# Kernel optimization log

Hardware: AMD Instinct MI355X
Metric: run time of the kernel (lower is better)

Reference implementation:

```python
import jax, jax.numpy as jnp
import numpy as np

STATE = 16
DT_RANK = 48
INNER = 1536
LN_EPS = 1e-5


def setup_inputs() -> dict:
    key = jax.random.key(0)
    ks = jax.random.split(key, 10)
    B, C, H, W = 128, 2048, 24, 12
    hid = 768
    inp = {}
    inp["x"] = jax.random.normal(ks[0], (B, C, H, W), jnp.float32)
    inp["pe_w"] = jax.random.normal(ks[1], (C, hid), jnp.float32) * 0.02
    inp["pe_b"] = jnp.zeros((hid,), jnp.float32)
    inp["ln_g"] = jnp.ones((hid,), jnp.float32)
    inp["ln_b"] = jnp.zeros((hid,), jnp.float32)
    inp["in_w"] = jax.random.normal(ks[2], (hid, 2 * INNER), jnp.float32) * 0.02
    inp["conv_w"] = jax.random.normal(ks[3], (INNER, 1, 3), jnp.float32) * 0.1
    inp["conv_b"] = jnp.zeros((INNER,), jnp.float32)
    # faithful init: A = repeat(arange(1, state+1)), A_log = log(A)
    inp["A_log"] = jnp.log(jnp.broadcast_to(jnp.arange(1, STATE + 1, dtype=jnp.float32), (INNER, STATE)))
    inp["xproj_w"] = jax.random.normal(ks[4], (INNER, DT_RANK + 2 * STATE), jnp.float32) * 0.02
    inp["dtproj_w"] = jax.random.normal(ks[5], (DT_RANK, INNER), jnp.float32) * 0.02
    inp["dtproj_b"] = jnp.zeros((INNER,), jnp.float32)
    inp["D_param"] = jnp.ones((INNER,), jnp.float32)
    inp["out_w"] = jax.random.normal(ks[6], (INNER, C), jnp.float32) * 0.02
    return inp


def _forward(x, pe_w, pe_b, ln_g, ln_b, in_w, conv_w, conv_b, A_log,
             xproj_w, dtproj_w, dtproj_b, D_param, out_w):
    B, C, H, W = x.shape
    # Patch_Embedding: AdaptiveAvgPool2d((3,3)) -- H,W divisible by 3 -> block mean
    xp = x.reshape(B, C, 3, H // 3, 3, W // 3).mean(axis=(3, 5))  # [B,C,3,3]
    tok = xp.reshape(B, C, 9).transpose(0, 2, 1)                   # [B,9,C]
    tok = tok @ pe_w + pe_b                                        # [B,9,hid]

    # Mamba: LayerNorm (biased variance)
    mu = tok.mean(-1, keepdims=True)
    var = tok.var(-1, keepdims=True)
    h = (tok - mu) / jnp.sqrt(var + LN_EPS) * ln_g + ln_b

    xz = h @ in_w                                                  # [B,9,2*inner]
    xs, z = xz[..., :INNER], xz[..., INNER:]

    # depthwise conv1d, kernel 3, pad 1
    xc = jax.lax.conv_general_dilated(
        xs.transpose(0, 2, 1), conv_w, window_strides=(1,), padding=[(1, 1)],
        feature_group_count=INNER, dimension_numbers=("NCH", "OIH", "NCH"))
    xc = (xc + conv_b[None, :, None]).transpose(0, 2, 1)           # [B,9,inner]
    xc = jax.nn.silu(xc)

    # SSM selective scan
    A = -jnp.exp(A_log)                                            # [inner,state]
    dbc = xc @ xproj_w                                             # [B,9,dtr+2*state]
    d_r = dbc[..., :DT_RANK]
    Bp = dbc[..., DT_RANK:DT_RANK + STATE]                         # [B,9,state]
    Cp = dbc[..., DT_RANK + STATE:]                                # [B,9,state]
    delta = jax.nn.softplus(d_r @ dtproj_w + dtproj_b)             # [B,9,inner]

    dA = jnp.exp(delta[..., None] * A)                             # [B,9,inner,state]
    dBu = delta[..., None] * Bp[:, :, None, :] * xc[..., None]     # [B,9,inner,state]

    def step(s, t):
        dA_i, dBu_i, C_i = t                                       # [B,inner,state],[B,inner,state],[B,state]
        s = dA_i * s + dBu_i
        y = jnp.einsum("bdn,bn->bd", s, C_i)
        return s, y

    s0 = jnp.zeros((B, INNER, STATE), xc.dtype)
    _, ys = jax.lax.scan(step, s0, (dA.transpose(1, 0, 2, 3),
                                    dBu.transpose(1, 0, 2, 3),
                                    Cp.transpose(1, 0, 2)))
    y = ys.transpose(1, 0, 2) + xc * D_param                       # [B,9,inner]

    y = y * jax.nn.silu(z)
    out = y @ out_w                                                # [B,9,C]

    # Inverse_Patch_Embedding: reshape to [B,C,3,3], bilinear upsample (align_corners=False)
    out = out.transpose(0, 2, 1).reshape(B, C, 3, 3)
    out = jax.image.resize(out, (B, C, H, W), method="bilinear")
    return out


def reference(x, pe_w, pe_b, ln_g, ln_b, in_w, conv_w, conv_b, A_log,
              xproj_w, dtproj_w, dtproj_b, D_param, out_w):
    return _forward(x, pe_w, pe_b, ln_g, ln_b, in_w, conv_w, conv_b, A_log,
                    xproj_w, dtproj_w, dtproj_b, D_param, out_w)
```

## Files before the change

### kernel.cpp

```cpp
#include <hip/hip_runtime.h>
#include <math.h>

#define Bn   128
#define Cn   2048
#define Hn   24
#define Wn   12
#define HID  768
#define NIN  1536
#define NST  16
#define DTR  48
#define Ln   9
#define Mn   (Bn*Ln)
#define XKS  16

typedef __bf16 bf16x8 __attribute__((ext_vector_type(8)));
typedef float  f32x4  __attribute__((ext_vector_type(4)));

#define GLOAD16(gsrc, ldst) \
  __builtin_amdgcn_global_load_lds((const __attribute__((address_space(1))) void*)(gsrc), \
                                   (__attribute__((address_space(3))) void*)(ldst), 16, 0, 0)

__device__ __forceinline__ unsigned short f2bf(float f) {
  unsigned u = __float_as_uint(f);
  u += 0x7fffu + ((u >> 16) & 1u);
  return (unsigned short)(u >> 16);
}
__device__ __forceinline__ float bf2f(unsigned short h) {
  return __uint_as_float(((unsigned)h) << 16);
}
__device__ __forceinline__ void split_bf(float f, unsigned short& hi, unsigned short& lo) {
  hi = f2bf(f);
  lo = f2bf(f - bf2f(hi));
}
__device__ __forceinline__ int col2(int k) { return ((k >> 5) << 6) + (k & 31); }

__global__ __launch_bounds__(256) void prep_kernel(const float* __restrict__ pe_w,
    const float* __restrict__ in_w, const float* __restrict__ out_w,
    const float* __restrict__ x,
    unsigned short* __restrict__ peT2, unsigned short* __restrict__ inT2,
    unsigned short* __restrict__ outT2, unsigned short* __restrict__ tok2) {
  __shared__ char smem[32 * 73 * 16];
  int bid = blockIdx.x;
  int t = threadIdx.x;
  if (bid < 6912) {
    float (*tile)[33] = reinterpret_cast<float (*)[33]>(smem);
    const float* W; unsigned short* T2; int K, N, nb, kb;
    if (bid < 1536)      { W = pe_w;  T2 = peT2;  K = Cn;  N = HID;     nb = bid % 24; kb = bid / 24; }
    else if (bid < 3840) { int q = bid - 1536; W = in_w;  T2 = inT2;  K = HID; N = 2 * NIN; nb = q % 96; kb = q / 96; }
    else                 { int q = bid - 3840; W = out_w; T2 = outT2; K = NIN; N = Cn;      nb = q % 64; kb = q / 64; }
    int kl = t >> 3, n4 = (t & 7) * 4;
    float4 v = *reinterpret_cast<const float4*>(W + (size_t)(kb * 32 + kl) * N + nb * 32 + n4);
    tile[kl][n4] = v.x; tile[kl][n4 + 1] = v.y; tile[kl][n4 + 2] = v.z; tile[kl][n4 + 3] = v.w;
    __syncthreads();
    int nl = t >> 3, k4 = (t & 7) * 4;
    unsigned short hi[4], lo[4];
    #pragma unroll
    for (int i = 0; i < 4; ++i) split_bf(tile[k4 + i][nl], hi[i], lo[i]);
    size_t base = (size_t)(nb * 32 + nl) * (2 * K) + kb * 64 + k4;
    uint2 ph, pl;
    ph.x = (unsigned)hi[0] | ((unsigned)hi[1] << 16);
    ph.y = (unsigned)hi[2] | ((unsigned)hi[3] << 16);
    pl.x = (unsigned)lo[0] | ((unsigned)lo[1] << 16);
    pl.y = (unsigned)lo[2] | ((unsigned)lo[3] << 16);
    *reinterpret_cast<uint2*>(T2 + base)      = ph;
    *reinterpret_cast<uint2*>(T2 + base + 32) = pl;
  } else {
    float4 (*raw)[73] = reinterpret_cast<float4 (*)[73]>(smem);
    int blk = bid - 6912;
    int b = blk >> 6, cg = blk & 63;
    const float4* src = reinterpret_cast<const float4*>(x) + (size_t)(b * Cn + cg * 32) * 72;
    #pragma unroll
    for (int it = 0; it < 9; ++it) {
      int li = it * 256 + t;
      raw[li / 72][li % 72] = src[li];
    }
    __syncthreads();
    for (int cell = t; cell < 288; cell += 256) {
      int c = cell / 9, p = cell % 9, i = p / 3, j = p % 3;
      float s = 0.f;
      #pragma unroll
      for (int k = 0; k < 8; ++k) {
        float4 v = raw[c][(i * 8 + k) * 3 + j];
        s += (v.x + v.y) + (v.z + v.w);
      }
      s *= (1.0f / 32.0f);
      unsigned short hi, lo;
      split_bf(s, hi, lo);
      int cglob = cg * 32 + c;
      size_t base = ((size_t)(b * Ln + p)) * (2 * Cn) + col2(cglob);
      tok2[base] = hi; tok2[base + 32] = lo;
    }
  }
}

__global__ __launch_bounds__(256) void mgemm_kernel(
    const unsigned short* __restrict__ A2, const unsigned short* __restrict__ B2,
    float* __restrict__ Cout, int M, int N, int K, int Ksub) {
  __shared__ unsigned short As[2][128][64];
  __shared__ unsigned short Bs[2][128][64];
  int t = threadIdx.x;
  int bm = blockIdx.y * 128, bn = blockIdx.x * 128;
  int wave = t >> 6, lane = t & 63;
  int wr = (wave >> 1) * 64, wc = (wave & 1) * 64;
  int lr = lane & 15, lk = lane >> 4;

  int l3 = lane >> 3, c8 = lane & 7;
  int sc = c8 ^ l3;
  size_t koff = (size_t)blockIdx.z * 2 * (size_t)Ksub;
  const unsigned short* Ab = A2 + (size_t)(bm + wave * 32 + l3) * (2 * (size_t)K) + koff + sc * 8;
  const unsigned short* Bb = B2 + (size_t)(bn + wave * 32 + l3) * (2 * (size_t)K) + koff + sc * 8;
  size_t rstep = (size_t)8 * 2 * K;

  f32x4 acc[4][4];
  #pragma unroll
  for (int m = 0; m < 4; ++m)
    #pragma unroll
    for (int n = 0; n < 4; ++n) acc[m][n] = {0.f, 0.f, 0.f, 0.f};

  {
    unsigned short* AsW = &As[0][wave * 32][0];
    unsigned short* BsW = &Bs[0][wave * 32][0];
    #pragma unroll
    for (int q = 0; q < 4; ++q) {
      GLOAD16(Ab + q * rstep, AsW + q * 8 * 64);
      GLOAD16(Bb + q * rstep, BsW + q * 8 * 64);
    }
  }
  __syncthreads();

  int cur = 0;
  for (int kk = 0; kk < Ksub; kk += 32) {
    if (kk + 32 < Ksub) {
      unsigned short* AsW = &As[cur ^ 1][wave * 32][0];
      unsigned short* BsW = &Bs[cur ^ 1][wave * 32][0];
      #pragma unroll
      for (int q = 0; q < 4; ++q) {
        GLOAD16(Ab + q * rstep + (kk + 32) * 2, AsW + q * 8 * 64);
        GLOAD16(Bb + q * rstep + (kk + 32) * 2, BsW + q * 8 * 64);
      }
    }

    bf16x8 ah[4], al[4], bh[4], bl[4];
    #pragma unroll
    for (int m = 0; m < 4; ++m) {
      int ar = wr + m * 16 + lr;
      ah[m] = *reinterpret_cast<const bf16x8*>(&As[cur][ar][((lk    ) ^ (ar & 7)) * 8]);
      al[m] = *reinterpret_cast<const bf16x8*>(&As[cur][ar][((4 + lk) ^ (ar & 7)) * 8]);
    }
    #pragma unroll
    for (int n = 0; n < 4; ++n) {
      int br = wc + n * 16 + lr;
      bh[n] = *reinterpret_cast<const bf16x8*>(&Bs[cur][br][((lk    ) ^ (br & 7)) * 8]);
      bl[n] = *reinterpret_cast<const bf16x8*>(&Bs[cur][br][((4 + lk) ^ (br & 7)) * 8]);
    }
    #pragma unroll
    for (int m = 0; m < 4; ++m)
      #pragma unroll
      for (int n = 0; n < 4; ++n) {
        acc[m][n] = __builtin_amdgcn_mfma_f32_16x16x32_bf16(ah[m], bh[n], acc[m][n], 0, 0, 0);
        acc[m][n] = __builtin_amdgcn_mfma_f32_16x16x32_bf16(ah[m], bl[n], acc[m][n], 0, 0, 0);
        acc[m][n] = __builtin_amdgcn_mfma_f32_16x16x32_bf16(al[m], bh[n], acc[m][n], 0, 0, 0);
      }
    __syncthreads();
    cur ^= 1;
  }

  float* dst = Cout + (size_t)blockIdx.z * M * N;
  #pragma unroll
  for (int m = 0; m < 4; ++m)
    #pragma unroll
    for (int n = 0; n < 4; ++n) {
      int col = bn + wc + n * 16 + lr;
      #pragma unroll
      for (int r = 0; r < 4; ++r) {
        int row = bm + wr + m * 16 + lk * 4 + r;
        dst[(size_t)row * N + col] = acc[m][n][r];
      }
    }
}

__global__ __launch_bounds__(256) void xproj_kernel(const float* __restrict__ xc,
    const float* __restrict__ w, float* __restrict__ part) {
  __shared__ float at[64][44];
  __shared__ float wt[32][80];
  int kc = blockIdx.x, mt = blockIdx.y;
  int t = threadIdx.x;
  int tx = t & 15, ty = t >> 4;
  float acc[4][5] = {};
  int sr = t >> 3, sc4 = (t & 7) * 4;
  for (int k0 = kc * 96; k0 < kc * 96 + 96; k0 += 32) {
    __syncthreads();
    float4 v0 = *reinterpret_cast<const float4*>(xc + (size_t)(mt * 64 + sr) * NIN + k0 + sc4);
    float4 v1 = *reinterpret_cast<const float4*>(xc + (size_t)(mt * 64 + sr + 32) * NIN + k0 + sc4);
    *reinterpret_cast<float4*>(&at[sr][sc4])      = v0;
    *reinterpret_cast<float4*>(&at[sr + 32][sc4]) = v1;
    for (int i = t; i < 32 * 80; i += 256)
      wt[i / 80][i % 80] = w[(size_t)(k0 + i / 80) * 80 + i % 80];
    __syncthreads();
    #pragma unroll
    for (int kk = 0; kk < 32; ++kk) {
      float a0[4], b0[5];
      #pragma unroll
      for (int i = 0; i < 4; ++i) a0[i] = at[ty * 4 + i][kk];
      #pragma unroll
      for (int j = 0; j < 5; ++j) b0[j] = wt[kk][tx + 16 * j];
      #pragma unroll
      for (int i = 0; i < 4; ++i)
        #pragma unroll
        for (int j = 0; j < 5; ++j)
          acc[i][j] = fmaf(a0[i], b0[j], acc[i][j]);
    }
  }
  #pragma unroll
  for (int i = 0; i < 4; ++i)
    #pragma unroll
    for (int j = 0; j < 5; ++j)
      part[((size_t)kc * Mn + mt * 64 + ty * 4 + i) * 80 + tx + 16 * j] = acc[i][j];
}

__global__ __launch_bounds__(256) void ln_kernel(const float* __restrict__ part1,
    const float* __restrict__ peb, const float* __restrict__ g, const float* __restrict__ be,
    unsigned short* __restrict__ h2) {
  int row = blockIdx.x;
  int t = threadIdx.x;
  float vq[3];
  #pragma unroll
  for (int q = 0; q < 3; ++q) {
    int c = t + q * 256;
    float v = peb[c];
    #pragma unroll
    for (int ks = 0; ks < 8; ++ks)
      v += part1[((size_t)ks * Mn + row) * HID + c];
    vq[q] = v;
  }
  float s  = vq[0] + vq[1] + vq[2];
  float s2 = vq[0] * vq[0] + vq[1] * vq[1] + vq[2] * vq[2];
  #pragma unroll
  for (int o = 32; o > 0; o >>= 1) {
    s  += __shfl_down(s,  o, 64);
    s2 += __shfl_down(s2, o, 64);
  }
  __shared__ float red[8];
  int wid = t >> 6, lane = t & 63;
  if (lane == 0) { red[wid] = s; red[4 + wid] = s2; }
  __syncthreads();
  float S  = red[0] + red[1] + red[2] + red[3];
  float S2 = red[4] + red[5] + red[6] + red[7];
  float mu  = S * (1.0f / HID);
  float var = S2 * (1.0f / HID) - mu * mu;
  float inv = rsqrtf(var + 1e-5f);
  #pragma unroll
  for (int q = 0; q < 3; ++q) {
    int c = t + q * 256;
    float hv = (vq[q] - mu) * inv * g[c] + be[c];
    unsigned short hi, lo;
    split_bf(hv, hi, lo);
    size_t base = (size_t)row * (2 * HID) + col2(c);
    h2[base] = hi; h2[base + 32] = lo;
  }
}

__global__ __launch_bounds__(256) void conv_silu_kernel(const float* __restrict__ part2,
    const float* __restrict__ w, const float* __restrict__ cb, float* __restrict__ xc) {
  int idx = blockIdx.x * 256 + threadIdx.x;
  if (idx >= Mn * NIN) return;
  int d  = idx % NIN;
  int bp = idx / NIN;
  int p = bp % Ln, b = bp / Ln;
  const float* pa = part2 + (size_t)(b * Ln) * (2 * NIN) + d;
  const float* pb = pa + (size_t)Mn * 2 * NIN;
  float acc = cb[d];
  float w0 = w[d * 3], w1 = w[d * 3 + 1], w2 = w[d * 3 + 2];
  if (p > 0) {
    size_t o1 = (size_t)(p - 1) * (2 * NIN);
    acc += (pa[o1] + pb[o1]) * w0;
  }
  size_t o2 = (size_t)p * (2 * NIN);
  acc += (pa[o2] + pb[o2]) * w1;
  if (p < Ln - 1) {
    size_t o3 = (size_t)(p + 1) * (2 * NIN);
    acc += (pa[o3] + pb[o3]) * w2;
  }
  float sg = 1.0f / (1.0f + expf(-acc));
  xc[idx] = acc * sg;
}

__global__ __launch_bounds__(256) void scan_kernel(const float* __restrict__ partx,
    const float* __restrict__ xcb, const float* __restrict__ A_log,
    const float* __restrict__ Dp, const float* __restrict__ part2,
    const float* __restrict__ dtw, const float* __restrict__ dtb,
    unsigned short* __restrict__ ya2) {
  __shared__ float wdt[DTR * 256];
  __shared__ float dbc9[Ln][DTR];
  __shared__ float Bsh[Ln][NST], Csh[Ln][NST];
  int b      = blockIdx.x / (NIN / 256);
  int dchunk = blockIdx.x % (NIN / 256);
  int t = threadIdx.x;
  float4* w4 = reinterpret_cast<float4*>(wdt);
  #pragma unroll
  for (int it = 0; it < 12; ++it) {
    int i4 = it * 256 + t;
    int k = i4 >> 6, c4 = i4 & 63;
    w4[i4] = *reinterpret_cast<const float4*>(dtw + (size_t)k * NIN + dchunk * 256 + c4 * 4);
  }
  for (int i = t; i < Ln * 80; i += 256) {
    int p = i / 80, k = i - p * 80;
    size_t off = (size_t)(b * Ln + p) * 80 + k;
    float s = 0.f;
    #pragma unroll
    for (int ks = 0; ks < XKS; ++ks) s += partx[(size_t)ks * (Mn * 80) + off];
    if (k < DTR)            dbc9[p][k] = s;
    else if (k < DTR + NST) Bsh[p][k - DTR] = s;
    else                    Csh[p][k - DTR - NST] = s;
  }
  __syncthreads();
  int d = dchunk * 256 + t;
  float Ar[NST];
  #pragma unroll
  for (int n = 0; n < NST; ++n) Ar[n] = -expf(A_log[(size_t)d * NST + n]);
  float s[NST];
  #pragma unroll
  for (int n = 0; n < NST; ++n) s[n] = 0.0f;
  float Dv = Dp[d];
  float bt = dtb[d];
  int cc = col2(d);
  const float* z0 = part2 + NIN + d;
  const float* z1 = z0 + (size_t)Mn * 2 * NIN;
  for (int p = 0; p < Ln; ++p) {
    size_t off = (size_t)(b * Ln + p) * NIN + d;
    float a = bt;
    #pragma unroll
    for (int k = 0; k < DTR; ++k) a = fmaf(dbc9[p][k], wdt[k * 256 + t], a);
    float dl = fmaxf(a, 0.0f) + log1pf(expf(-fabsf(a)));
    float u  = xcb[off];
    float du = dl * u;
    float y = 0.0f;
    #pragma unroll
    for (int n = 0; n < NST; ++n) {
      float dA = expf(dl * Ar[n]);
      s[n] = dA * s[n] + du * Bsh[p][n];
      y += s[n] * Csh[p][n];
    }
    size_t zoff = (size_t)(b * Ln + p) * (2 * NIN);
    float zv = z0[zoff] + z1[zoff];
    float sz = zv / (1.0f + expf(-zv));
    float yv = (y + u * Dv) * sz;
    unsigned short hi, lo;
    split_bf(yv, hi, lo);
    size_t base = (size_t)(b * Ln + p) * (2 * NIN) + cc;
    ya2[base] = hi; ya2[base + 32] = lo;
  }
}

__global__ __launch_bounds__(256) void resize_kernel(const float* __restrict__ part3,
                                                     float* __restrict__ out) {
  __shared__ float v[32][10];
  int blk = blockIdx.x;
  int b = blk >> 6, cg = blk & 63;
  int t = threadIdx.x;
  size_t MN3 = (size_t)Mn * Cn;
  for (int i = t; i < 288; i += 256) {
    int p = i >> 5, c = i & 31;
    size_t base = (size_t)(b * Ln + p) * Cn + cg * 32 + c;
    v[c][p] = part3[base] + part3[base + MN3] + part3[base + 2 * MN3] + part3[base + 3 * MN3];
  }
  __syncthreads();
  int ch = t >> 3, sub = t & 7;
  float* dst = out + ((size_t)b * Cn + cg * 32 + ch) * 288;
  #pragma unroll
  for (int q = 0; q < 9; ++q) {
    int f = sub + q * 8;
    int y = f / 3, xq = f - y * 3;
    float fy  = (y + 0.5f) * 0.125f - 0.5f;
    float fyf = floorf(fy);
    float wy  = fy - fyf;
    int yy = (int)fyf;
    int y0 = min(2, max(0, yy)), y1 = min(2, max(0, yy + 1));
    float rr[3];
    #pragma unroll
    for (int j = 0; j < 3; ++j)
      rr[j] = v[ch][y0 * 3 + j] * (1.0f - wy) + v[ch][y1 * 3 + j] * wy;
    float ov[4];
    #pragma unroll
    for (int xi = 0; xi < 4; ++xi) {
      int xo = xq * 4 + xi;
      float fx  = (xo + 0.5f) * 0.25f - 0.5f;
      float fxf = floorf(fx);
      float wx  = fx - fxf;
      int xx = (int)fxf;
      int x0 = min(2, max(0, xx)), x1 = min(2, max(0, xx + 1));
      ov[xi] = rr[x0] * (1.0f - wx) + rr[x1] * wx;
    }
    *reinterpret_cast<float4*>(dst + f * 4) = make_float4(ov[0], ov[1], ov[2], ov[3]);
  }
}

extern "C" void kernel_launch(void* const* d_in, const int* in_sizes, int n_in,
                              void* d_out, int out_size, void* d_ws, size_t ws_size,
                              hipStream_t stream) {
  const float* x        = (const float*)d_in[0];
  const float* pe_w     = (const float*)d_in[1];
  const float* pe_b     = (const float*)d_in[2];
  const float* ln_g     = (const float*)d_in[3];
  const float* ln_b     = (const float*)d_in[4];
  const float* in_w     = (const float*)d_in[5];
  const float* conv_w   = (const float*)d_in[6];
  const float* conv_b   = (const float*)d_in[7];
  const float* A_log    = (const float*)d_in[8];
  const float* xproj_w  = (const float*)d_in[9];
  const float* dtproj_w = (const float*)d_in[10];
  const float* dtproj_b = (const float*)d_in[11];
  const float* D_param  = (const float*)d_in[12];
  const float* out_w    = (const float*)d_in[13];
  float* out = (float*)d_out;
  char* ws = (char*)d_ws;

  size_t o = 0;
  auto alloc = [&](size_t bytes) { size_t r = o; o += (bytes + 255) & ~(size_t)255; return r; };
  unsigned short* tok2  = (unsigned short*)(ws + alloc((size_t)Mn * 2 * Cn * 2));
  unsigned short* peT2  = (unsigned short*)(ws + alloc((size_t)HID * 2 * Cn * 2));
  unsigned short* inT2  = (unsigned short*)(ws + alloc((size_t)2 * NIN * 2 * HID * 2));
  unsigned short* outT2 = (unsigned short*)(ws + alloc((size_t)Cn * 2 * NIN * 2));
  unsigned short* h2    = (unsigned short*)(ws + alloc((size_t)Mn * 2 * HID * 2));
  unsigned short* ya2   = (unsigned short*)(ws + alloc((size_t)Mn * 2 * NIN * 2));
  float* xc    = (float*)(ws + alloc((size_t)Mn * NIN * 4));
  float* part1 = (float*)(ws + alloc((size_t)8 * Mn * HID * 4));
  float* part2 = (float*)(ws + alloc((size_t)2 * Mn * 2 * NIN * 4));
  float* part3 = (float*)(ws + alloc((size_t)4 * Mn * Cn * 4));
  float* partx = (float*)(ws + alloc((size_t)XKS * Mn * 80 * 4));

  prep_kernel<<<15104, 256, 0, stream>>>(pe_w, in_w, out_w, x, peT2, inT2, outT2, tok2);

  mgemm_kernel<<<dim3(HID / 128, Mn / 128, 8), 256, 0, stream>>>(
      tok2, peT2, part1, Mn, HID, Cn, Cn / 8);
  ln_kernel<<<Mn, 256, 0, stream>>>(part1, pe_b, ln_g, ln_b, h2);
  mgemm_kernel<<<dim3(2 * NIN / 128, Mn / 128, 2), 256, 0, stream>>>(
      h2, inT2, part2, Mn, 2 * NIN, HID, HID / 2);
  conv_silu_kernel<<<(Mn * NIN) / 256, 256, 0, stream>>>(part2, conv_w, conv_b, xc);
  xproj_kernel<<<dim3(XKS, Mn / 64), 256, 0, stream>>>(xc, xproj_w, partx);
  scan_kernel<<<Bn * (NIN / 256), 256, 0, stream>>>(
      partx, xc, A_log, D_param, part2, dtproj_w, dtproj_b, ya2);
  mgemm_kernel<<<dim3(Cn / 128, Mn / 128, 4), 256, 0, stream>>>(
      ya2, outT2, part3, Mn, Cn, NIN, NIN / 4);
  resize_kernel<<<Bn * (Cn / 32), 256, 0, stream>>>(part3, out);
}
```

Before: 312.3 us.

## Fuse depthwise conv+SiLU into xproj and scan, halve out-proj split-K

Removes the standalone conv_silu kernel and its xc buffer. The depthwise conv and SiLU are now recomputed on the fly from the in-projection partials, both inside the xproj GEMM tile loader and inside the scan kernel, which slides a three-tap window along the sequence. It also switches expf to __expf in the scan, and reduces the output GEMM split-K from 4 to 2, which shrinks the partial buffer the resize kernel reads. The cost is redundant conv work and extra partial-buffer reads in xproj and scan, plus fewer blocks for the output GEMM.

```diff
diff --git a/kernel.cpp b/kernel.cpp
--- a/kernel.cpp
+++ b/kernel.cpp
@@ -179,7 +179,42 @@
     }
 }
 
-__global__ __launch_bounds__(256) void xproj_kernel(const float* __restrict__ xc,
+__device__ __forceinline__ float4 conv_silu4(const float* __restrict__ p0,
+    const float* __restrict__ p1, const float* __restrict__ cw,
+    const float* __restrict__ cb, int R, int d0) {
+  int bq = R / 9, pq = R - bq * 9;
+  size_t rb = (size_t)R * (2 * NIN) + d0;
+  float4 a0 = *reinterpret_cast<const float4*>(p0 + rb);
+  float4 a1 = *reinterpret_cast<const float4*>(p1 + rb);
+  float cx[4] = {a0.x + a1.x, a0.y + a1.y, a0.z + a1.z, a0.w + a1.w};
+  float cm[4] = {0.f, 0.f, 0.f, 0.f}, cp[4] = {0.f, 0.f, 0.f, 0.f};
+  if (pq > 0) {
+    float4 m0 = *reinterpret_cast<const float4*>(p0 + rb - 2 * NIN);
+    float4 m1 = *reinterpret_cast<const float4*>(p1 + rb - 2 * NIN);
+    cm[0] = m0.x + m1.x; cm[1] = m0.y + m1.y; cm[2] = m0.z + m1.z; cm[3] = m0.w + m1.w;
+  }
+  if (pq < Ln - 1) {
+    float4 q0 = *reinterpret_cast<const float4*>(p0 + rb + 2 * NIN);
+    float4 q1 = *reinterpret_cast<const float4*>(p1 + rb + 2 * NIN);
+    cp[0] = q0.x + q1.x; cp[1] = q0.y + q1.y; cp[2] = q0.z + q1.z; cp[3] = q0.w + q1.w;
+  }
+  float4 w0 = *reinterpret_cast<const float4*>(cw + 3 * d0);
+  float4 w1 = *reinterpret_cast<const float4*>(cw + 3 * d0 + 4);
+  float4 w2 = *reinterpret_cast<const float4*>(cw + 3 * d0 + 8);
+  float wf[12] = {w0.x, w0.y, w0.z, w0.w, w1.x, w1.y, w1.z, w1.w, w2.x, w2.y, w2.z, w2.w};
+  float4 cb4 = *reinterpret_cast<const float4*>(cb + d0);
+  float cbf[4] = {cb4.x, cb4.y, cb4.z, cb4.w};
+  float r[4];
+  #pragma unroll
+  for (int i = 0; i < 4; ++i) {
+    float a = cbf[i] + cm[i] * wf[3 * i] + cx[i] * wf[3 * i + 1] + cp[i] * wf[3 * i + 2];
+    r[i] = a / (1.0f + __expf(-a));
+  }
+  return make_float4(r[0], r[1], r[2], r[3]);
+}
+
+__global__ __launch_bounds__(256) void xproj_kernel(const float* __restrict__ part2,
+    const float* __restrict__ cw, const float* __restrict__ cb,
     const float* __restrict__ w, float* __restrict__ part) {
   __shared__ float at[64][44];
   __shared__ float wt[32][80];
@@ -188,10 +223,12 @@
   int tx = t & 15, ty = t >> 4;
   float acc[4][5] = {};
   int sr = t >> 3, sc4 = (t & 7) * 4;
+  const float* p0 = part2;
+  const float* p1 = part2 + (size_t)Mn * 2 * NIN;
   for (int k0 = kc * 96; k0 < kc * 96 + 96; k0 += 32) {
+    float4 v0 = conv_silu4(p0, p1, cw, cb, mt * 64 + sr,      k0 + sc4);
+    float4 v1 = conv_silu4(p0, p1, cw, cb, mt * 64 + sr + 32, k0 + sc4);
     __syncthreads();
-    float4 v0 = *reinterpret_cast<const float4*>(xc + (size_t)(mt * 64 + sr) * NIN + k0 + sc4);
-    float4 v1 = *reinterpret_cast<const float4*>(xc + (size_t)(mt * 64 + sr + 32) * NIN + k0 + sc4);
     *reinterpret_cast<float4*>(&at[sr][sc4])      = v0;
     *reinterpret_cast<float4*>(&at[sr + 32][sc4]) = v1;
     for (int i = t; i < 32 * 80; i += 256)
@@ -260,36 +297,11 @@
   }
 }
 
-__global__ __launch_bounds__(256) void conv_silu_kernel(const float* __restrict__ part2,
-    const float* __restrict__ w, const float* __restrict__ cb, float* __restrict__ xc) {
-  int idx = blockIdx.x * 256 + threadIdx.x;
-  if (idx >= Mn * NIN) return;
-  int d  = idx % NIN;
-  int bp = idx / NIN;
-  int p = bp % Ln, b = bp / Ln;
-  const float* pa = part2 + (size_t)(b * Ln) * (2 * NIN) + d;
-  const float* pb = pa + (size_t)Mn * 2 * NIN;
-  float acc = cb[d];
-  float w0 = w[d * 3], w1 = w[d * 3 + 1], w2 = w[d * 3 + 2];
-  if (p > 0) {
-    size_t o1 = (size_t)(p - 1) * (2 * NIN);
-    acc += (pa[o1] + pb[o1]) * w0;
-  }
-  size_t o2 = (size_t)p * (2 * NIN);
-  acc += (pa[o2] + pb[o2]) * w1;
-  if (p < Ln - 1) {
-    size_t o3 = (size_t)(p + 1) * (2 * NIN);
-    acc += (pa[o3] + pb[o3]) * w2;
-  }
-  float sg = 1.0f / (1.0f + expf(-acc));
-  xc[idx] = acc * sg;
-}
-
 __global__ __launch_bounds__(256) void scan_kernel(const float* __restrict__ partx,
-    const float* __restrict__ xcb, const float* __restrict__ A_log,
-    const float* __restrict__ Dp, const float* __restrict__ part2,
-    const float* __restrict__ dtw, const float* __restrict__ dtb,
-    unsigned short* __restrict__ ya2) {
+    const float* __restrict__ A_log, const float* __restrict__ Dp,
+    const float* __restrict__ part2, const float* __restrict__ dtw,
+    const float* __restrict__ dtb, const float* __restrict__ cw,
+    const float* __restrict__ cb, unsigned short* __restrict__ ya2) {
   __shared__ float wdt[DTR * 256];
   __shared__ float dbc9[Ln][DTR];
   __shared__ float Bsh[Ln][NST], Csh[Ln][NST];
@@ -317,38 +329,47 @@
   int d = dchunk * 256 + t;
   float Ar[NST];
   #pragma unroll
-  for (int n = 0; n < NST; ++n) Ar[n] = -expf(A_log[(size_t)d * NST + n]);
+  for (int n = 0; n < NST; ++n) Ar[n] = -__expf(A_log[(size_t)d * NST + n]);
   float s[NST];
   #pragma unroll
   for (int n = 0; n < NST; ++n) s[n] = 0.0f;
   float Dv = Dp[d];
   float bt = dtb[d];
+  float w0 = cw[3 * d], w1 = cw[3 * d + 1], w2 = cw[3 * d + 2];
+  float cbv = cb[d];
   int cc = col2(d);
-  const float* z0 = part2 + NIN + d;
-  const float* z1 = z0 + (size_t)Mn * 2 * NIN;
+  const float* px0 = part2 + d;
+  const float* px1 = px0 + (size_t)Mn * 2 * NIN;
+  const float* z0  = part2 + NIN + d;
+  const float* z1  = z0 + (size_t)Mn * 2 * NIN;
+  size_t row0 = (size_t)(b * Ln) * (2 * NIN);
+  float xm = 0.f;
+  float x0 = px0[row0] + px1[row0];
   for (int p = 0; p < Ln; ++p) {
-    size_t off = (size_t)(b * Ln + p) * NIN + d;
+    size_t roff = row0 + (size_t)p * (2 * NIN);
+    float xp = 0.f;
+    if (p < Ln - 1) xp = px0[roff + 2 * NIN] + px1[roff + 2 * NIN];
+    float a0 = cbv + xm * w0 + x0 * w1 + xp * w2;
+    float u = a0 / (1.0f + __expf(-a0));
     float a = bt;
     #pragma unroll
     for (int k = 0; k < DTR; ++k) a = fmaf(dbc9[p][k], wdt[k * 256 + t], a);
-    float dl = fmaxf(a, 0.0f) + log1pf(expf(-fabsf(a)));
-    float u  = xcb[off];
+    float dl = fmaxf(a, 0.0f) + log1pf(__expf(-fabsf(a)));
     float du = dl * u;
     float y = 0.0f;
     #pragma unroll
     for (int n = 0; n < NST; ++n) {
-      float dA = expf(dl * Ar[n]);
+      float dA = __expf(dl * Ar[n]);
       s[n] = dA * s[n] + du * Bsh[p][n];
       y += s[n] * Csh[p][n];
     }
-    size_t zoff = (size_t)(b * Ln + p) * (2 * NIN);
-    float zv = z0[zoff] + z1[zoff];
-    float sz = zv / (1.0f + expf(-zv));
+    float zv = z0[roff] + z1[roff];
+    float sz = zv / (1.0f + __expf(-zv));
     float yv = (y + u * Dv) * sz;
     unsigned short hi, lo;
     split_bf(yv, hi, lo);
-    size_t base = (size_t)(b * Ln + p) * (2 * NIN) + cc;
-    ya2[base] = hi; ya2[base + 32] = lo;
+    ya2[roff + cc] = hi; ya2[roff + cc + 32] = lo;
+    xm = x0; x0 = xp;
   }
 }
 
@@ -362,7 +383,7 @@
   for (int i = t; i < 288; i += 256) {
     int p = i >> 5, c = i & 31;
     size_t base = (size_t)(b * Ln + p) * Cn + cg * 32 + c;
-    v[c][p] = part3[base] + part3[base + MN3] + part3[base + 2 * MN3] + part3[base + 3 * MN3];
+    v[c][p] = part3[base] + part3[base + MN3];
   }
   __syncthreads();
   int ch = t >> 3, sub = t & 7;
@@ -423,10 +444,9 @@
   unsigned short* outT2 = (unsigned short*)(ws + alloc((size_t)Cn * 2 * NIN * 2));
   unsigned short* h2    = (unsigned short*)(ws + alloc((size_t)Mn * 2 * HID * 2));
   unsigned short* ya2   = (unsigned short*)(ws + alloc((size_t)Mn * 2 * NIN * 2));
-  float* xc    = (float*)(ws + alloc((size_t)Mn * NIN * 4));
   float* part1 = (float*)(ws + alloc((size_t)8 * Mn * HID * 4));
   float* part2 = (float*)(ws + alloc((size_t)2 * Mn * 2 * NIN * 4));
-  float* part3 = (float*)(ws + alloc((size_t)4 * Mn * Cn * 4));
+  float* part3 = (float*)(ws + alloc((size_t)2 * Mn * Cn * 4));
   float* partx = (float*)(ws + alloc((size_t)XKS * Mn * 80 * 4));
 
   prep_kernel<<<15104, 256, 0, stream>>>(pe_w, in_w, out_w, x, peT2, inT2, outT2, tok2);
@@ -436,11 +456,10 @@
   ln_kernel<<<Mn, 256, 0, stream>>>(part1, pe_b, ln_g, ln_b, h2);
   mgemm_kernel<<<dim3(2 * NIN / 128, Mn / 128, 2), 256, 0, stream>>>(
       h2, inT2, part2, Mn, 2 * NIN, HID, HID / 2);
-  conv_silu_kernel<<<(Mn * NIN) / 256, 256, 0, stream>>>(part2, conv_w, conv_b, xc);
-  xproj_kernel<<<dim3(XKS, Mn / 64), 256, 0, stream>>>(xc, xproj_w, partx);
+  xproj_kernel<<<dim3(XKS, Mn / 64), 256, 0, stream>>>(part2, conv_w, conv_b, xproj_w, partx);
   scan_kernel<<<Bn * (NIN / 256), 256, 0, stream>>>(
-      partx, xc, A_log, D_param, part2, dtproj_w, dtproj_b, ya2);
-  mgemm_kernel<<<dim3(Cn / 128, Mn / 128, 4), 256, 0, stream>>>(
-      ya2, outT2, part3, Mn, Cn, NIN, NIN / 4);
+      partx, A_log, D_param, part2, dtproj_w, dtproj_b, conv_w, conv_b, ya2);
+  mgemm_kernel<<<dim3(Cn / 128, Mn / 128, 2), 256, 0, stream>>>(
+      ya2, outT2, part3, Mn, Cn, NIN, NIN / 2);
   resize_kernel<<<Bn * (Cn / 32), 256, 0, stream>>>(part3, out);
 }
```

After: 302.4 us. 1.03x faster.
